# Kernel optimization log

Hardware: AMD Instinct MI355X
Metric: run time of the kernel (lower is better)

## Reference

```python
import jax, jax.numpy as jnp
from jax import lax
import numpy as np

SHAPE = (64, 64, 64)  # spatial grid (D, H, W)
N_PTS = 100000        # active voxels
KPAD = (1, 2, 2)      # 'same' padding for (3,5,5) kernel


def _conv(x, w, pad):
    # x: [B,D,H,W,C], w: [kd,kh,kw,Cin,Cout]
    return lax.conv_general_dilated(
        x, w, window_strides=(1, 1, 1),
        padding=[(p, p) for p in pad],
        dimension_numbers=('NDHWC', 'DHWIO', 'NDHWC'))


def _sparse_maxpool2(x, mask):
    # spconv SparseMaxPool3d(2,2): output active where any input in 2x2x2
    # window is active; value = max over active inputs only.
    neg = jnp.float32(-1e30)
    xm = jnp.where(mask > 0, x, neg)
    win = (1, 2, 2, 2, 1)
    y = lax.reduce_window(xm, neg, lax.max, win, win, 'VALID')
    m2 = lax.reduce_window(mask, jnp.float32(0), lax.max, win, win, 'VALID')
    return jnp.where(m2 > 0, y, 0.0), m2


def setup_inputs() -> dict:
    rng = np.random.default_rng(0)
    D, H, W = SHAPE
    lin = rng.choice(D * H * W, size=N_PTS, replace=False)  # unique voxels
    z = lin // (H * W)
    y = (lin // W) % H
    x = lin % W
    coors = np.stack([np.zeros(N_PTS, np.int32), z, y, x], 1).astype(np.int32)

    key = jax.random.key(0)
    ks = jax.random.split(key, 16)
    feats = jax.random.normal(ks[0], (N_PTS, 3), jnp.float32)

    dims = [(3, 64), (64, 64), (64, 96), (96, 96), (96, 128), (128, 128),
            (128, 160), (160, 160), (160, 192), (192, 192), (192, 224),
            (224, 224), (224, 256), (256, 256)]
    inp = {'features': feats, 'coors': jnp.asarray(coors), 'batch_size': 1}
    for i, (ci, co) in enumerate(dims):
        scale = 1.0 / np.sqrt(ci * 75.0)  # 75 = 3*5*5 kernel taps
        inp[f'w{i}'] = jax.random.normal(ks[i + 1], (3, 5, 5, ci, co),
                                         jnp.float32) * scale
    return inp


def reference(features, coors, batch_size,
              w0, w1, w2, w3, w4, w5, w6, w7, w8, w9, w10, w11, w12, w13):
    # Densify the sparse tensor: inactive voxels are exactly zero, so a dense
    # conv followed by masking to the active set reproduces submanifold conv.
    b, z, y, x = coors[:, 0], coors[:, 1], coors[:, 2], coors[:, 3]
    dense = jnp.zeros((1,) + SHAPE + (3,), jnp.float32).at[b, z, y, x].set(features)
    mask = jnp.zeros((1,) + SHAPE + (1,), jnp.float32).at[b, z, y, x].set(1.0)

    ws = [w0, w1, w2, w3, w4, w5, w6, w7, w8, w9, w10, w11]
    h = dense
    wi = 0
    for _lvl in range(6):  # 6 (subm, subm, pool2) stages
        h = _conv(h, ws[wi], KPAD) * mask; wi += 1
        h = _conv(h, ws[wi], KPAD) * mask; wi += 1
        h, mask = _sparse_maxpool2(h, mask)

    # SparseConv3d(224,256,(3,5,5),padding=(1,2,2)): output active set is the
    # dilation of the input active set by the kernel footprint.
    m2 = lax.reduce_window(mask, jnp.float32(0), lax.max,
                           (1, 3, 5, 5, 1), (1, 1, 1, 1, 1),
                           [(0, 0), (1, 1), (2, 2), (2, 2), (0, 0)])
    h = _conv(h, w12, KPAD) * m2
    mask = m2
    # final SubMConv3d(256,256)
    h = _conv(h, w13, KPAD) * mask
    return h  # [1,1,1,1,256]
```

## Files before the change

kernel.cpp:

```cpp
#include <hip/hip_runtime.h>
#include <hip/hip_bf16.h>
#include <cstdint>

typedef __attribute__((ext_vector_type(8))) short bf16x8;
typedef __attribute__((ext_vector_type(4))) float f32x4;

__device__ __forceinline__ unsigned short f2bf_hi(float v) {
    unsigned u = __float_as_uint(v);
    u = u + 0x7fffu + ((u >> 16) & 1u);
    return (unsigned short)(u >> 16);
}
__device__ __forceinline__ float bf2f(unsigned short h) {
    return __uint_as_float(((unsigned)h) << 16);
}

__global__ void scatter_kernel(const float* __restrict__ feats,
                               const int* __restrict__ coors,
                               float* __restrict__ dense,
                               float* __restrict__ mask, int n)
{
    int i = blockIdx.x * blockDim.x + threadIdx.x;
    if (i >= n) return;
    const int z = coors[i * 4 + 1];
    const int y = coors[i * 4 + 2];
    const int x = coors[i * 4 + 3];
    const size_t s = (size_t)((z * 64 + y) * 64 + x);
    dense[s * 3 + 0] = feats[i * 3 + 0];
    dense[s * 3 + 1] = feats[i * 3 + 1];
    dense[s * 3 + 2] = feats[i * 3 + 2];
    mask[s] = 1.f;
}

__global__ void wprep_kernel(const float* __restrict__ w,
                             unsigned short* __restrict__ wv, int CI, int CO)
{
    const int total = 75 * CI * CO;
    const int stride = gridDim.x * blockDim.x;
    for (int i = blockIdx.x * blockDim.x + threadIdx.x; i < total; i += stride) {
        const int tap = i / (CI * CO);
        const int r = i - tap * CI * CO;
        const int ci = r / CO;
        const int co = r - ci * CO;
        const size_t o = ((size_t)(tap * (CI / 8) + (ci >> 3)) * CO + co) * 8 + (ci & 7);
        wv[o] = f2bf_hi(w[i]);
    }
}

__global__ void wprep2_kernel(const float* __restrict__ w,
                              unsigned short* __restrict__ wv, int CI, int CO)
{
    const int total = 75 * CI * CO;
    const int stride = gridDim.x * blockDim.x;
    for (int i = blockIdx.x * blockDim.x + threadIdx.x; i < total; i += stride) {
        const int tap = i / (CI * CO);
        const int r = i - tap * CI * CO;
        const int ci = r / CO;
        const int co = r - ci * CO;
        const float v = w[i];
        const unsigned short h = f2bf_hi(v);
        const unsigned short l = f2bf_hi(v - bf2f(h));
        const size_t o = ((size_t)(tap * (CI / 8) + (ci >> 3)) * CO + co) * 16 + (ci & 7);
        wv[o] = h; wv[o + 8] = l;
    }
}

__global__ __launch_bounds__(256)
void conv1_kernel(const float* __restrict__ in, const float* __restrict__ w,
                  const float* __restrict__ mask, unsigned short* __restrict__ ob)
{
    constexpr int S = 64, SP = 68;
    __shared__ float lds[15][3][SP];

    const int bid = blockIdx.y * S + blockIdx.x;
    const int wg = (bid & 7) * (S * S / 8) + (bid >> 3);
    const int y = wg & 63, z = wg >> 6;
    const int t = threadIdx.x;

    for (int idx = t; idx < 15 * 3 * SP; idx += 256) {
        const int r = idx / (3 * SP);
        const int rem = idx - r * 3 * SP;
        const int ci = rem / SP;
        const int x = rem - ci * SP;
        const int kz = r / 5, ky = r - kz * 5;
        const int zz = z + kz - 1, yy = y + ky - 2, xi = x - 2;
        float v = 0.f;
        if ((unsigned)zz < (unsigned)S && (unsigned)yy < (unsigned)S && (unsigned)xi < (unsigned)S)
            v = in[(size_t)((zz * S + yy) * S + xi) * 3 + ci];
        lds[r][ci][x] = v;
    }
    __syncthreads();

    const int co = t & 63, xs = t >> 6;
    float acc[16];
#pragma unroll
    for (int i = 0; i < 16; ++i) acc[i] = 0.f;

#pragma unroll 1
    for (int r = 0; r < 15; ++r) {
#pragma unroll
        for (int ci = 0; ci < 3; ++ci) {
            float inv[20];
#pragma unroll
            for (int j = 0; j < 5; ++j)
                *(float4*)&inv[j * 4] = *(const float4*)&lds[r][ci][xs * 16 + j * 4];
            const float* wp = w + (size_t)(r * 15 + ci) * 64 + co;
#pragma unroll
            for (int kx = 0; kx < 5; ++kx) {
                const float wv = wp[kx * 192];
#pragma unroll
                for (int i = 0; i < 16; ++i) acc[i] += inv[i + kx] * wv;
            }
        }
    }

    const size_t vb = (size_t)(z * S + y) * S;
#pragma unroll
    for (int i = 0; i < 16; ++i) {
        const int x = xs * 16 + i;
        const float keep = (mask[vb + x] > 0.f) ? 1.f : 0.f;
        ob[(vb + x) * 64 + co] = f2bf_hi(acc[i] * keep);
    }
}

template<int CIN, int COUT, int S, int YB, int YG, int WN, int NG, int OMODE>
__global__ __launch_bounds__(YG * NG * 64)
void mfma_conv7(const unsigned short* __restrict__ ab,
                const unsigned short* __restrict__ wv,
                const float* __restrict__ mask, float* __restrict__ outf,
                unsigned short* __restrict__ outb)
{
    constexpr int SP = S + 4;
    constexpr int MX = S / 16;
    constexpr int KC = CIN / 32;
    constexpr int KC4 = CIN / 8;
    constexpr int RS = (KC4 <= 8) ? 8 : 16;
    constexpr int PLANE = SP * RS;
    constexpr int NLR = SP * KC4;
    constexpr int NL = 2 * NLR;
    constexpr int NW = YG * NG;
    constexpr int NT = NW * 64;
    constexpr int SREG = (NL + NT - 1) / NT;
    constexpr int YBW = YB / YG;
    constexpr int NYB = S / YB;
    constexpr int JP = (YB + 4) / 2;
    constexpr int NP = 3 * JP;
    static_assert(COUT / 16 == WN * NG, "geometry");
    static_assert((YB + 4) % 2 == 0, "YB even");

    __shared__ unsigned short lds[2 * 2 * PLANE * 8];

    const int bid = blockIdx.y * NYB + blockIdx.x;
    constexpr int NWG = NYB * S;
    const int wg = (bid & 7) * (NWG / 8) + (bid >> 3);
    const int yb = wg % NYB, z = wg / NYB;
    const int y0 = yb * YB;

    const int t = threadIdx.x;
    const int lane = t & 63;
    const int wave = t >> 6;
    const int waveN = wave % NG;
    const int waveY = wave / NG;
    const int col = lane & 15;
    const int ci8 = lane >> 4;

    f32x4 acc[YBW][MX][WN];
    const f32x4 vzero = {0.f, 0.f, 0.f, 0.f};
#pragma unroll
    for (int q = 0; q < YBW; ++q)
#pragma unroll
        for (int m = 0; m < MX; ++m)
#pragma unroll
            for (int n = 0; n < WN; ++n) acc[q][m][n] = vzero;

    uint4 reg[SREG];

    auto issue = [&](int ph) {
        const int kz = ph / JP, jp = ph - kz * JP;
        const int zz = z + kz - 1;
        const bool zv = ((unsigned)zz < (unsigned)S);
#pragma unroll
        for (int i = 0; i < SREG; ++i) {
            const int L = i * NT + t;
            uint4 v = {0u, 0u, 0u, 0u};
            if (L < NL) {
                const int jr = L / NLR;
                const int l2 = L - jr * NLR;
                const int x = l2 / KC4;
                const int c3 = l2 - x * KC4;
                const int xi = x - 2;
                const int yy = y0 + jp * 2 + jr - 2;
                if (zv && (unsigned)yy < (unsigned)S && (unsigned)xi < (unsigned)S)
                    v = *(const uint4*)(ab + (size_t)((zz * S + yy) * S + xi) * CIN + c3 * 8);
            }
            reg[i] = v;
        }
    };
    auto store = [&](int pl) {
#pragma unroll
        for (int i = 0; i < SREG; ++i) {
            const int L = i * NT + t;
            if (L < NL) {
                const int jr = L / NLR;
                const int l2 = L - jr * NLR;
                const int x = l2 / KC4;
                const int c3 = l2 - x * KC4;
                const int p = x * RS + (c3 ^ (x & 7));
                *(uint4*)&lds[((pl * 2 + jr) * PLANE + p) * 8] = reg[i];
            }
        }
    };

    issue(0);
    store(0);
    if (NP > 1) issue(1);
    __syncthreads();

    int cur = 0;
#pragma unroll 1
    for (int ph = 0; ph < NP; ++ph) {
        const int kz = ph / JP, jp = ph - kz * JP;
        const int zz = z + kz - 1;
        if ((unsigned)zz < (unsigned)S) {
#pragma unroll
            for (int jr = 0; jr < 2; ++jr) {
                const int j = jp * 2 + jr;
                const int yy = y0 + j - 2;
                if ((unsigned)yy >= (unsigned)S) continue;
                const unsigned short* plane = lds + (cur * 2 + jr) * PLANE * 8;

                bool vq[YBW];
                int tapb[YBW];
#pragma unroll
                for (int ql = 0; ql < YBW; ++ql) {
                    const int q = waveY * YBW + ql;
                    const int ky = j - q;
                    vq[ql] = (ky >= 0 && ky <= 4);
                    tapb[ql] = (kz * 5 + (vq[ql] ? ky : 0)) * 5;
                }

                bf16x8 wA[YBW][KC][WN], wB[YBW][KC][WN];
                auto wload = [&](bf16x8 (&wb)[YBW][KC][WN], int kx) {
#pragma unroll
                    for (int ql = 0; ql < YBW; ++ql) if (vq[ql]) {
                        const int tap = tapb[ql] + kx;
#pragma unroll
                        for (int kc = 0; kc < KC; ++kc) {
                            const int c3 = kc * 4 + ci8;
#pragma unroll
                            for (int n = 0; n < WN; ++n) {
                                const int co = (waveN * WN + n) * 16 + col;
                                wb[ql][kc][n] = *(const bf16x8*)(wv + ((size_t)(tap * KC4 + c3) * COUT + co) * 8);
                            }
                        }
                    }
                };
                auto wmfma = [&](bf16x8 (&wb)[YBW][KC][WN], bf16x8 (&a)[KC][MX]) {
#pragma unroll
                    for (int ql = 0; ql < YBW; ++ql) if (vq[ql])
#pragma unroll
                        for (int kc = 0; kc < KC; ++kc)
#pragma unroll
                            for (int m = 0; m < MX; ++m)
#pragma unroll
                                for (int n = 0; n < WN; ++n)
                                    acc[ql][m][n] = __builtin_amdgcn_mfma_f32_16x16x32_bf16(a[kc][m], wb[ql][kc][n], acc[ql][m][n], 0, 0, 0);
                };

                wload(wA, 0);
                __builtin_amdgcn_s_setprio(1);
#pragma unroll
                for (int kx = 0; kx < 5; ++kx) {
                    bf16x8 a[KC][MX];
#pragma unroll
                    for (int kc = 0; kc < KC; ++kc) {
                        const int c3 = kc * 4 + ci8;
#pragma unroll
                        for (int m = 0; m < MX; ++m) {
                            const int x = m * 16 + col + kx;
                            const int p = x * RS + (c3 ^ (x & 7));
                            a[kc][m] = *(const bf16x8*)&plane[p * 8];
                        }
                    }
                    if ((kx & 1) == 0) {
                        if (kx + 1 < 5) wload(wB, kx + 1);
                        wmfma(wA, a);
                    } else {
                        if (kx + 1 < 5) wload(wA, kx + 1);
                        wmfma(wB, a);
                    }
                }
                __builtin_amdgcn_s_setprio(0);
            }
        }
        if (ph + 1 < NP) store(cur ^ 1);
        if (ph + 2 < NP) issue(ph + 2);
        __syncthreads();
        cur ^= 1;
    }

    const int rq = lane >> 4;
#pragma unroll
    for (int ql = 0; ql < YBW; ++ql) {
        const int y = y0 + waveY * YBW + ql;
        const size_t vb = (size_t)(z * S + y) * S;
#pragma unroll
        for (int m = 0; m < MX; ++m) {
            const int xb = m * 16 + rq * 4;
#pragma unroll
            for (int r = 0; r < 4; ++r) {
                const int x = xb + r;
                const float keep = (mask[vb + x] > 0.f) ? 1.f : 0.f;
#pragma unroll
                for (int n = 0; n < WN; ++n) {
                    const int co = (waveN * WN + n) * 16 + col;
                    const float v = acc[ql][m][n][r] * keep;
                    if (OMODE == 0) outf[(vb + x) * COUT + co] = v;
                    else            outb[(vb + x) * COUT + co] = f2bf_hi(v);
                }
            }
        }
    }
}

template<int CIN, int COUT, int S, int WM, int WN, int MG, int NG, int OMODE>
__global__ __launch_bounds__(MG * NG * 64)
void mfma_conv3c(const unsigned short* __restrict__ ab,
                 const unsigned short* __restrict__ wv,
                 const float* __restrict__ mask, float* __restrict__ outf,
                 unsigned short* __restrict__ outb)
{
    constexpr int SP = S + 4;
    constexpr int KC = CIN / 32;
    constexpr int KC4 = CIN / 8;
    constexpr int RS = (KC4 <= 8) ? 8 : 16;
    constexpr int PLANE = SP * RS;
    constexpr int NL = SP * KC4;
    constexpr int NT = MG * NG * 64;
    constexpr int SREG = (NL + NT - 1) / NT;
    static_assert(S / 16 == WM * MG && COUT / 16 == WN * NG, "geometry");

    __shared__ unsigned short lds[2 * PLANE * 8];

    const int bid = blockIdx.y * S + blockIdx.x;
    const int wg = (bid & 7) * (S * S / 8) + (bid >> 3);
    const int y = wg % S, z = wg / S;

    const int t = threadIdx.x;
    const int lane = t & 63;
    const int wave = t >> 6;
    const int waveM = wave % MG;
    const int waveN = wave / MG;
    const int col = lane & 15;
    const int ci8 = lane >> 4;

    f32x4 acc[WM][WN];
    const f32x4 vzero = {0.f, 0.f, 0.f, 0.f};
#pragma unroll
    for (int m = 0; m < WM; ++m)
#pragma unroll
        for (int n = 0; n < WN; ++n) acc[m][n] = vzero;

    uint4 reg[SREG];

    auto issue = [&](int kzy) {
        const int kz = kzy / 5, ky = kzy - kz * 5;
        const int zz = z + kz - 1, yy = y + ky - 2;
        const bool rv = ((unsigned)zz < (unsigned)S) && ((unsigned)yy < (unsigned)S);
        const size_t rowbase = rv ? (size_t)((zz * S + yy) * S) * CIN : 0;
#pragma unroll
        for (int i = 0; i < SREG; ++i) {
            const int L = i * NT + t;
            uint4 v = {0u, 0u, 0u, 0u};
            if (L < NL) {
                const int x = L / KC4;
                const int c3 = L - x * KC4;
                const int xi = x - 2;
                if (rv && (unsigned)xi < (unsigned)S)
                    v = *(const uint4*)(ab + rowbase + (size_t)xi * CIN + c3 * 8);
            }
            reg[i] = v;
        }
    };
    auto store = [&](int pl) {
#pragma unroll
        for (int i = 0; i < SREG; ++i) {
            const int L = i * NT + t;
            if (L < NL) {
                const int x = L / KC4;
                const int c3 = L - x * KC4;
                const int p = x * RS + (c3 ^ (x & 7));
                *(uint4*)&lds[(pl * PLANE + p) * 8] = reg[i];
            }
        }
    };

    issue(0);
    store(0);
    issue(1);
    __syncthreads();

    int cur = 0;
#pragma unroll 1
    for (int kzy = 0; kzy < 15; ++kzy) {
        const int kz = kzy / 5, ky = kzy - kz * 5;
        const int zz = z + kz - 1, yy = y + ky - 2;
        if (((unsigned)zz < (unsigned)S) && ((unsigned)yy < (unsigned)S)) {
            const unsigned short* plane = lds + cur * PLANE * 8;

            bf16x8 wA[KC][WN], wB[KC][WN];
            auto wload = [&](bf16x8 (&wb)[KC][WN], int kx) {
                const int tap = kzy * 5 + kx;
#pragma unroll
                for (int kc = 0; kc < KC; ++kc) {
                    const int c3 = kc * 4 + ci8;
#pragma unroll
                    for (int n = 0; n < WN; ++n) {
                        const int co = (waveN * WN + n) * 16 + col;
                        wb[kc][n] = *(const bf16x8*)(wv + ((size_t)(tap * KC4 + c3) * COUT + co) * 8);
                    }
                }
            };
            auto wmfma = [&](bf16x8 (&wb)[KC][WN], bf16x8 (&a)[KC][WM]) {
#pragma unroll
                for (int kc = 0; kc < KC; ++kc)
#pragma unroll
                    for (int m = 0; m < WM; ++m)
#pragma unroll
                        for (int n = 0; n < WN; ++n)
                            acc[m][n] = __builtin_amdgcn_mfma_f32_16x16x32_bf16(a[kc][m], wb[kc][n], acc[m][n], 0, 0, 0);
            };

            wload(wA, 0);
            __builtin_amdgcn_s_setprio(1);
#pragma unroll
            for (int kx = 0; kx < 5; ++kx) {
                bf16x8 a[KC][WM];
#pragma unroll
                for (int kc = 0; kc < KC; ++kc) {
                    const int c3 = kc * 4 + ci8;
#pragma unroll
                    for (int m = 0; m < WM; ++m) {
                        const int x = (waveM * WM + m) * 16 + col + kx;
                        const int p = x * RS + (c3 ^ (x & 7));
                        a[kc][m] = *(const bf16x8*)&plane[p * 8];
                    }
                }
                if ((kx & 1) == 0) {
                    if (kx + 1 < 5) wload(wB, kx + 1);
                    wmfma(wA, a);
                } else {
                    if (kx + 1 < 5) wload(wA, kx + 1);
                    wmfma(wB, a);
                }
            }
            __builtin_amdgcn_s_setprio(0);
        }
        if (kzy + 1 < 15) store(cur ^ 1);
        if (kzy + 2 < 15) issue(kzy + 2);
        __syncthreads();
        cur ^= 1;
    }

    const int rq = lane >> 4;
    const size_t vb = (size_t)(z * S + y) * S;
#pragma unroll
    for (int m = 0; m < WM; ++m) {
        const int xb = (waveM * WM + m) * 16 + rq * 4;
#pragma unroll
        for (int r = 0; r < 4; ++r) {
            const int x = xb + r;
            const float keep = (mask[vb + x] > 0.f) ? 1.f : 0.f;
#pragma unroll
            for (int n = 0; n < WN; ++n) {
                const int co = (waveN * WN + n) * 16 + col;
                const float v = acc[m][n][r] * keep;
                if (OMODE == 0) outf[(vb + x) * COUT + co] = v;
                else            outb[(vb + x) * COUT + co] = f2bf_hi(v);
            }
        }
    }
}

template<int CIN, int COUT, int S, int NW>
__global__ __launch_bounds__(NW * 64)
void dgemm2_kernel(const unsigned short* __restrict__ inb,
                   const unsigned short* __restrict__ wv,
                   const float* __restrict__ mask,
                   unsigned short* __restrict__ outb)
{
    constexpr int M = S * S * S;
    constexpr int KC = CIN / 32;
    constexpr int KC4 = CIN / 8;
    __shared__ f32x4 part[NW][64];

    const int t = threadIdx.x;
    const int lane = t & 63;
    const int w = t >> 6;
    const int col = lane & 15;
    const int g = lane >> 4;

    const int va = blockIdx.x * 16 + col;
    const bool av = (va < M);
    const int az = (va / (S * S)) % S;
    const int ay = (va / S) % S;
    const int ax = va % S;
    const int co = blockIdx.y * 16 + col;

    f32x4 acc0 = {0.f, 0.f, 0.f, 0.f};
    f32x4 acc1 = {0.f, 0.f, 0.f, 0.f};

#pragma unroll 2
    for (int tap = w; tap < 75; tap += NW) {
        const int dz = tap / 25 - 1;
        const int dy = (tap / 5) % 5 - 2;
        const int dx = tap % 5 - 2;
        const int zz = az + dz, yy = ay + dy, xx = ax + dx;
        const bool valid = av && ((unsigned)zz < (unsigned)S) &&
                           ((unsigned)yy < (unsigned)S) && ((unsigned)xx < (unsigned)S);
        const size_t abase = valid ? (size_t)((zz * S + yy) * S + xx) * CIN : 0;
#pragma unroll
        for (int kc = 0; kc < KC; ++kc) {
            const int c3 = kc * 4 + g;
            bf16x8 a = {0, 0, 0, 0, 0, 0, 0, 0};
            if (valid) a = *(const bf16x8*)(inb + abase + c3 * 8);
            const unsigned short* wp = wv + ((size_t)(tap * KC4 + c3) * COUT + co) * 16;
            bf16x8 wh = *(const bf16x8*)wp;
            bf16x8 wl = *(const bf16x8*)(wp + 8);
            acc0 = __builtin_amdgcn_mfma_f32_16x16x32_bf16(a, wh, acc0, 0, 0, 0);
            acc1 = __builtin_amdgcn_mfma_f32_16x16x32_bf16(a, wl, acc1, 0, 0, 0);
        }
    }

    part[w][lane] = acc0 + acc1;
    __syncthreads();

    if (w == 0) {
        f32x4 s = part[0][lane];
#pragma unroll
        for (int i = 1; i < NW; ++i) s += part[i][lane];
#pragma unroll
        for (int r = 0; r < 4; ++r) {
            const int v = blockIdx.x * 16 + g * 4 + r;
            if (v < M) {
                const float keep = (mask[v] > 0.f) ? 1.f : 0.f;
                outb[(size_t)v * COUT + co] = f2bf_hi(s[r] * keep);
            }
        }
    }
}

__global__ void pool_bf8_kernel(const unsigned short* __restrict__ inb,
                                const float* __restrict__ mi,
                                unsigned short* __restrict__ outb,
                                float* __restrict__ mo, int S, int C)
{
    const int So = S >> 1;
    const int C8 = C >> 3;
    const long long total = (long long)So * So * So * C8;
    for (long long i = blockIdx.x * (long long)blockDim.x + threadIdx.x; i < total;
         i += (long long)gridDim.x * blockDim.x) {
        const int c8 = (int)(i % C8);
        const long long s = i / C8;
        const int xo = (int)(s % So);
        const int yo = (int)((s / So) % So);
        const int zo = (int)(s / ((long long)So * So));
        float best[8];
#pragma unroll
        for (int k = 0; k < 8; ++k) best[k] = -1e30f;
        float m2 = 0.f;
        for (int dz = 0; dz < 2; ++dz)
            for (int dy = 0; dy < 2; ++dy)
                for (int dx = 0; dx < 2; ++dx) {
                    const int zi = zo * 2 + dz, yi = yo * 2 + dy, xi = xo * 2 + dx;
                    const float m = mi[(zi * S + yi) * S + xi];
                    if (m > 0.f) {
                        m2 = 1.f;
                        const unsigned short* p =
                            inb + ((size_t)((zi * S + yi) * S + xi) * C8 + c8) * 8;
                        uint4 v = *(const uint4*)p;
                        const unsigned short* vs = (const unsigned short*)&v;
#pragma unroll
                        for (int k = 0; k < 8; ++k) best[k] = fmaxf(best[k], bf2f(vs[k]));
                    }
                }
        uint4 o;
        unsigned short* os = (unsigned short*)&o;
#pragma unroll
        for (int k = 0; k < 8; ++k) os[k] = f2bf_hi((m2 > 0.f) ? best[k] : 0.f);
        *(uint4*)(outb + i * 8) = o;
        if (c8 == 0) mo[s] = m2;
    }
}

__global__ __launch_bounds__(256)
void final_kernel(const unsigned short* __restrict__ h, const float* __restrict__ mask,
                  const float* __restrict__ w12, const float* __restrict__ w13,
                  float* __restrict__ out)
{
    __shared__ float o1[256];
    const int co = threadIdx.x;
    const float m = (mask[0] > 0.f) ? 1.f : 0.f;
    float a = 0.f;
    for (int ci = 0; ci < 224; ++ci)
        a += bf2f(h[ci]) * w12[(size_t)(37 * 224 + ci) * 256 + co];
    o1[co] = a * m;
    __syncthreads();
    float b = 0.f;
    for (int ci = 0; ci < 256; ++ci)
        b += o1[ci] * w13[(size_t)(37 * 256 + ci) * 256 + co];
    out[co] = b * m;
}

static void pool_bf8(const unsigned short* inb, const float* mi,
                     unsigned short* outb, float* mo, int S, int C, hipStream_t stream)
{
    const long long total = (long long)(S / 2) * (S / 2) * (S / 2) * (C / 8);
    long long grid = (total + 255) / 256;
    if (grid > 4096) grid = 4096;
    if (grid < 1) grid = 1;
    pool_bf8_kernel<<<(int)grid, 256, 0, stream>>>(inb, mi, outb, mo, S, C);
}

#define WOFF0 0
#define WOFF1 307200
#define WOFF2 768000
#define WOFF3 1459200
#define WOFF4 2380800
#define DOFF6 0
#define DOFF7 3072000
#define DOFF8 6912000
#define DOFF9 11520000
#define DOFF10 17049600
#define DOFF11 23500800

extern "C" void kernel_launch(void* const* d_in, const int* in_sizes, int n_in,
                              void* d_out, int out_size, void* d_ws, size_t ws_size,
                              hipStream_t stream)
{
    const float* feats = (const float*)d_in[0];
    const int*   coors = (const int*)d_in[1];
    const float* w[14];
    for (int i = 0; i < 14; ++i) w[i] = (const float*)d_in[3 + i];
    float* outp = (float*)d_out;

    float* dense0 = (float*)d_ws;
    float* mA = dense0 + 786432;
    float* mB = mA + 262144;
    unsigned short* ab = (unsigned short*)(mB + 262144);
    unsigned short* bb = ab + 16777216;
    unsigned short* wvp = bb + 16777216;
    unsigned short* wdp = wvp + 3609600;

    const int npts = in_sizes[0] / 3;

    wprep_kernel<<<256, 256, 0, stream>>>(w[1], wvp + WOFF0, 64, 64);
    wprep_kernel<<<256, 256, 0, stream>>>(w[2], wvp + WOFF1, 64, 96);
    wprep_kernel<<<256, 256, 0, stream>>>(w[3], wvp + WOFF2, 96, 96);
    wprep_kernel<<<256, 256, 0, stream>>>(w[4], wvp + WOFF3, 96, 128);
    wprep_kernel<<<256, 256, 0, stream>>>(w[5], wvp + WOFF4, 128, 128);
    wprep2_kernel<<<256, 256, 0, stream>>>(w[6], wdp + DOFF6, 128, 160);
    wprep2_kernel<<<256, 256, 0, stream>>>(w[7], wdp + DOFF7, 160, 160);
    wprep2_kernel<<<256, 256, 0, stream>>>(w[8], wdp + DOFF8, 160, 192);
    wprep2_kernel<<<256, 256, 0, stream>>>(w[9], wdp + DOFF9, 192, 192);
    wprep2_kernel<<<256, 256, 0, stream>>>(w[10], wdp + DOFF10, 192, 224);
    wprep2_kernel<<<256, 256, 0, stream>>>(w[11], wdp + DOFF11, 224, 224);

    hipMemsetAsync(dense0, 0, (size_t)786432 * sizeof(float), stream);
    hipMemsetAsync(mA, 0, (size_t)262144 * sizeof(float), stream);
    scatter_kernel<<<(npts + 255) / 256, 256, 0, stream>>>(feats, coors, dense0, mA, npts);

    conv1_kernel<<<dim3(64, 64), 256, 0, stream>>>(dense0, w[0], mA, ab);
    mfma_conv7<64, 64, 64, 4, 2, 2, 2, 1><<<dim3(16, 64), 256, 0, stream>>>(
        ab, wvp + WOFF0, mA, nullptr, bb);
    pool_bf8(bb, mA, ab, mB, 64, 64, stream);
    mfma_conv7<64, 96, 32, 4, 2, 3, 2, 1><<<dim3(8, 32), 256, 0, stream>>>(
        ab, wvp + WOFF1, mB, nullptr, bb);
    mfma_conv7<96, 96, 32, 4, 2, 3, 2, 1><<<dim3(8, 32), 256, 0, stream>>>(
        bb, wvp + WOFF2, mB, nullptr, ab);
    pool_bf8(ab, mB, bb, mA, 32, 96, stream);
    mfma_conv3c<96, 128, 16, 1, 2, 1, 4, 1><<<dim3(16, 16), 256, 0, stream>>>(
        bb, wvp + WOFF3, mA, nullptr, ab);
    mfma_conv3c<128, 128, 16, 1, 2, 1, 4, 1><<<dim3(16, 16), 256, 0, stream>>>(
        ab, wvp + WOFF4, mA, nullptr, bb);
    pool_bf8(bb, mA, ab, mB, 16, 128, stream);
    dgemm2_kernel<128, 160, 8, 4><<<dim3(32, 10), 256, 0, stream>>>(ab, wdp + DOFF6, mB, bb);
    dgemm2_kernel<160, 160, 8, 4><<<dim3(32, 10), 256, 0, stream>>>(bb, wdp + DOFF7, mB, ab);
    pool_bf8(ab, mB, bb, mA, 8, 160, stream);
    dgemm2_kernel<160, 192, 4, 8><<<dim3(4, 12), 512, 0, stream>>>(bb, wdp + DOFF8, mA, ab);
    dgemm2_kernel<192, 192, 4, 8><<<dim3(4, 12), 512, 0, stream>>>(ab, wdp + DOFF9, mA, bb);
    pool_bf8(bb, mA, ab, mB, 4, 192, stream);
    dgemm2_kernel<192, 224, 2, 8><<<dim3(1, 14), 512, 0, stream>>>(ab, wdp + DOFF10, mB, bb);
    dgemm2_kernel<224, 224, 2, 8><<<dim3(1, 14), 512, 0, stream>>>(bb, wdp + DOFF11, mB, ab);
    pool_bf8(ab, mB, bb, mA, 2, 224, stream);
    final_kernel<<<1, 256, 0, stream>>>(bb, mA, w[12], w[13], outp);
}
```

Before: 865.0 us.

## Replace conv3c with y-blocked conv6 kernel reusing input rows across outputs

Replaces the per-(z,y) row conv kernel with a version where each workgroup computes several adjacent y rows. Each staged input row plane is reused for every output row whose 5-tap y window covers it, which cuts redundant input loads and barriers. The 32^3 stages now use this new kernel with 2 rows per block, and the 16^3 stages switch to the existing mfma_conv7 with different tiling. The cost is more accumulator registers per wave and some wasted phases at the block edges, where invalid taps are skipped.

```diff
diff --git a/kernel.cpp b/kernel.cpp
--- a/kernel.cpp
+++ b/kernel.cpp
@@ -322,49 +322,58 @@
     }
 }
 
-template<int CIN, int COUT, int S, int WM, int WN, int MG, int NG, int OMODE>
-__global__ __launch_bounds__(MG * NG * 64)
-void mfma_conv3c(const unsigned short* __restrict__ ab,
-                 const unsigned short* __restrict__ wv,
-                 const float* __restrict__ mask, float* __restrict__ outf,
-                 unsigned short* __restrict__ outb)
+template<int CIN, int COUT, int S, int YB, int YG, int WN, int NG, int OMODE>
+__global__ __launch_bounds__(YG * NG * 64)
+void mfma_conv6(const unsigned short* __restrict__ ab,
+                const unsigned short* __restrict__ wv,
+                const float* __restrict__ mask, float* __restrict__ outf,
+                unsigned short* __restrict__ outb)
 {
     constexpr int SP = S + 4;
+    constexpr int MX = S / 16;
     constexpr int KC = CIN / 32;
     constexpr int KC4 = CIN / 8;
     constexpr int RS = (KC4 <= 8) ? 8 : 16;
     constexpr int PLANE = SP * RS;
     constexpr int NL = SP * KC4;
-    constexpr int NT = MG * NG * 64;
+    constexpr int NW = YG * NG;
+    constexpr int NT = NW * 64;
     constexpr int SREG = (NL + NT - 1) / NT;
-    static_assert(S / 16 == WM * MG && COUT / 16 == WN * NG, "geometry");
+    constexpr int YBW = YB / YG;
+    constexpr int NYB = S / YB;
+    constexpr int NP = 3 * (YB + 4);
+    static_assert(COUT / 16 == WN * NG, "geometry");
 
     __shared__ unsigned short lds[2 * PLANE * 8];
 
-    const int bid = blockIdx.y * S + blockIdx.x;
-    const int wg = (bid & 7) * (S * S / 8) + (bid >> 3);
-    const int y = wg % S, z = wg / S;
+    const int bid = blockIdx.y * NYB + blockIdx.x;
+    constexpr int NWG = NYB * S;
+    const int wg = (bid & 7) * (NWG / 8) + (bid >> 3);
+    const int yb = wg % NYB, z = wg / NYB;
+    const int y0 = yb * YB;
 
     const int t = threadIdx.x;
     const int lane = t & 63;
     const int wave = t >> 6;
-    const int waveM = wave % MG;
-    const int waveN = wave / MG;
+    const int waveN = wave % NG;
+    const int waveY = wave / NG;
     const int col = lane & 15;
     const int ci8 = lane >> 4;
 
-    f32x4 acc[WM][WN];
+    f32x4 acc[YBW][MX][WN];
     const f32x4 vzero = {0.f, 0.f, 0.f, 0.f};
 #pragma unroll
-    for (int m = 0; m < WM; ++m)
-#pragma unroll
-        for (int n = 0; n < WN; ++n) acc[m][n] = vzero;
+    for (int q = 0; q < YBW; ++q)
+#pragma unroll
+        for (int m = 0; m < MX; ++m)
+#pragma unroll
+            for (int n = 0; n < WN; ++n) acc[q][m][n] = vzero;
 
     uint4 reg[SREG];
 
-    auto issue = [&](int kzy) {
-        const int kz = kzy / 5, ky = kzy - kz * 5;
-        const int zz = z + kz - 1, yy = y + ky - 2;
+    auto issue = [&](int ph) {
+        const int kz = ph / (YB + 4), j = ph - kz * (YB + 4);
+        const int zz = z + kz - 1, yy = y0 + j - 2;
         const bool rv = ((unsigned)zz < (unsigned)S) && ((unsigned)yy < (unsigned)S);
         const size_t rowbase = rv ? (size_t)((zz * S + yy) * S) * CIN : 0;
 #pragma unroll
@@ -396,51 +405,66 @@
 
     issue(0);
     store(0);
-    issue(1);
+    if (NP > 1) issue(1);
     __syncthreads();
 
     int cur = 0;
 #pragma unroll 1
-    for (int kzy = 0; kzy < 15; ++kzy) {
-        const int kz = kzy / 5, ky = kzy - kz * 5;
-        const int zz = z + kz - 1, yy = y + ky - 2;
+    for (int ph = 0; ph < NP; ++ph) {
+        const int kz = ph / (YB + 4), j = ph - kz * (YB + 4);
+        const int zz = z + kz - 1, yy = y0 + j - 2;
         if (((unsigned)zz < (unsigned)S) && ((unsigned)yy < (unsigned)S)) {
             const unsigned short* plane = lds + cur * PLANE * 8;
 
-            bf16x8 wA[KC][WN], wB[KC][WN];
-            auto wload = [&](bf16x8 (&wb)[KC][WN], int kx) {
-                const int tap = kzy * 5 + kx;
-#pragma unroll
-                for (int kc = 0; kc < KC; ++kc) {
-                    const int c3 = kc * 4 + ci8;
-#pragma unroll
-                    for (int n = 0; n < WN; ++n) {
-                        const int co = (waveN * WN + n) * 16 + col;
-                        wb[kc][n] = *(const bf16x8*)(wv + ((size_t)(tap * KC4 + c3) * COUT + co) * 8);
+            bool vq[YBW];
+            int tapb[YBW];
+#pragma unroll
+            for (int ql = 0; ql < YBW; ++ql) {
+                const int q = waveY * YBW + ql;
+                const int ky = j - q;
+                vq[ql] = (ky >= 0 && ky <= 4);
+                tapb[ql] = (kz * 5 + (vq[ql] ? ky : 0)) * 5;
+            }
+
+            bf16x8 wA[YBW][KC][WN], wB[YBW][KC][WN];
+            auto wload = [&](bf16x8 (&wb)[YBW][KC][WN], int kx) {
+#pragma unroll
+                for (int ql = 0; ql < YBW; ++ql) if (vq[ql]) {
+                    const int tap = tapb[ql] + kx;
+#pragma unroll
+                    for (int kc = 0; kc < KC; ++kc) {
+                        const int c3 = kc * 4 + ci8;
+#pragma unroll
+                        for (int n = 0; n < WN; ++n) {
+                            const int co = (waveN * WN + n) * 16 + col;
+                            wb[ql][kc][n] = *(const bf16x8*)(wv + ((size_t)(tap * KC4 + c3) * COUT + co) * 8);
+                        }
                     }
                 }
             };
-            auto wmfma = [&](bf16x8 (&wb)[KC][WN], bf16x8 (&a)[KC][WM]) {
-#pragma unroll
-                for (int kc = 0; kc < KC; ++kc)
-#pragma unroll
-                    for (int m = 0; m < WM; ++m)
-#pragma unroll
-                        for (int n = 0; n < WN; ++n)
-                            acc[m][n] = __builtin_amdgcn_mfma_f32_16x16x32_bf16(a[kc][m], wb[kc][n], acc[m][n], 0, 0, 0);
+            auto wmfma = [&](bf16x8 (&wb)[YBW][KC][WN], bf16x8 (&a)[KC][MX]) {
+#pragma unroll
+                for (int ql = 0; ql < YBW; ++ql) if (vq[ql])
+#pragma unroll
+                    for (int kc = 0; kc < KC; ++kc)
+#pragma unroll
+                        for (int m = 0; m < MX; ++m)
+#pragma unroll
+                            for (int n = 0; n < WN; ++n)
+                                acc[ql][m][n] = __builtin_amdgcn_mfma_f32_16x16x32_bf16(a[kc][m], wb[ql][kc][n], acc[ql][m][n], 0, 0, 0);
             };
 
             wload(wA, 0);
             __builtin_amdgcn_s_setprio(1);
 #pragma unroll
             for (int kx = 0; kx < 5; ++kx) {
-                bf16x8 a[KC][WM];
+                bf16x8 a[KC][MX];
 #pragma unroll
                 for (int kc = 0; kc < KC; ++kc) {
                     const int c3 = kc * 4 + ci8;
 #pragma unroll
-                    for (int m = 0; m < WM; ++m) {
-                        const int x = (waveM * WM + m) * 16 + col + kx;
+                    for (int m = 0; m < MX; ++m) {
+                        const int x = m * 16 + col + kx;
                         const int p = x * RS + (c3 ^ (x & 7));
                         a[kc][m] = *(const bf16x8*)&plane[p * 8];
                     }
@@ -455,27 +479,31 @@
             }
             __builtin_amdgcn_s_setprio(0);
         }
-        if (kzy + 1 < 15) store(cur ^ 1);
-        if (kzy + 2 < 15) issue(kzy + 2);
+        if (ph + 1 < NP) store(cur ^ 1);
+        if (ph + 2 < NP) issue(ph + 2);
         __syncthreads();
         cur ^= 1;
     }
 
     const int rq = lane >> 4;
-    const size_t vb = (size_t)(z * S + y) * S;
-#pragma unroll
-    for (int m = 0; m < WM; ++m) {
-        const int xb = (waveM * WM + m) * 16 + rq * 4;
-#pragma unroll
-        for (int r = 0; r < 4; ++r) {
-            const int x = xb + r;
-            const float keep = (mask[vb + x] > 0.f) ? 1.f : 0.f;
-#pragma unroll
-            for (int n = 0; n < WN; ++n) {
-                const int co = (waveN * WN + n) * 16 + col;
-                const float v = acc[m][n][r] * keep;
-                if (OMODE == 0) outf[(vb + x) * COUT + co] = v;
-                else            outb[(vb + x) * COUT + co] = f2bf_hi(v);
+#pragma unroll
+    for (int ql = 0; ql < YBW; ++ql) {
+        const int y = y0 + waveY * YBW + ql;
+        const size_t vb = (size_t)(z * S + y) * S;
+#pragma unroll
+        for (int m = 0; m < MX; ++m) {
+            const int xb = m * 16 + rq * 4;
+#pragma unroll
+            for (int r = 0; r < 4; ++r) {
+                const int x = xb + r;
+                const float keep = (mask[vb + x] > 0.f) ? 1.f : 0.f;
+#pragma unroll
+                for (int n = 0; n < WN; ++n) {
+                    const int co = (waveN * WN + n) * 16 + col;
+                    const float v = acc[ql][m][n][r] * keep;
+                    if (OMODE == 0) outf[(vb + x) * COUT + co] = v;
+                    else            outb[(vb + x) * COUT + co] = f2bf_hi(v);
+                }
             }
         }
     }
@@ -673,14 +701,14 @@
     mfma_conv7<64, 64, 64, 4, 2, 2, 2, 1><<<dim3(16, 64), 256, 0, stream>>>(
         ab, wvp + WOFF0, mA, nullptr, bb);
     pool_bf8(bb, mA, ab, mB, 64, 64, stream);
-    mfma_conv7<64, 96, 32, 4, 2, 3, 2, 1><<<dim3(8, 32), 256, 0, stream>>>(
+    mfma_conv6<64, 96, 32, 2, 1, 2, 3, 1><<<dim3(16, 32), 192, 0, stream>>>(
         ab, wvp + WOFF1, mB, nullptr, bb);
-    mfma_conv7<96, 96, 32, 4, 2, 3, 2, 1><<<dim3(8, 32), 256, 0, stream>>>(
+    mfma_conv6<96, 96, 32, 2, 1, 2, 3, 1><<<dim3(16, 32), 192, 0, stream>>>(
         bb, wvp + WOFF2, mB, nullptr, ab);
     pool_bf8(ab, mB, bb, mA, 32, 96, stream);
-    mfma_conv3c<96, 128, 16, 1, 2, 1, 4, 1><<<dim3(16, 16), 256, 0, stream>>>(
+    mfma_conv7<96, 128, 16, 2, 1, 2, 4, 1><<<dim3(8, 16), 256, 0, stream>>>(
         bb, wvp + WOFF3, mA, nullptr, ab);
-    mfma_conv3c<128, 128, 16, 1, 2, 1, 4, 1><<<dim3(16, 16), 256, 0, stream>>>(
+    mfma_conv7<128, 128, 16, 2, 1, 2, 4, 1><<<dim3(8, 16), 256, 0, stream>>>(
         ab, wvp + WOFF4, mA, nullptr, bb);
     pool_bf8(bb, mA, ab, mB, 16, 128, stream);
     dgemm2_kernel<128, 160, 8, 4><<<dim3(32, 10), 256, 0, stream>>>(ab, wdp + DOFF6, mB, bb);
```

Result: no change. 871.9 us (+0.8%).
